# Kernel tuning notes

Measured on AMD Instinct MI355X. Metric: run time of the kernel, lower is better.

The kernel has to match this reference:

```python
import jax, jax.numpy as jnp
import numpy as np

N_NODES = 50000
N_EDGES = 800000
IN_CH = 128
HID = 32
HEADS = 4
OUT_CH = 64
NEG_SLOPE = 0.2
EPS = 1e-16


def setup_inputs() -> dict:
    key = jax.random.key(0)
    ks = jax.random.split(key, 12)
    x = jax.random.normal(ks[0], (N_NODES, IN_CH), dtype=jnp.float32)
    edge_index = jax.random.randint(ks[1], (2, N_EDGES), 0, N_NODES, dtype=jnp.int32)
    s1 = 1.0 / np.sqrt(IN_CH)
    s2 = 1.0 / np.sqrt(HEADS * HID)
    W1 = jax.random.uniform(ks[2], (IN_CH, HEADS * HID), jnp.float32, -s1, s1)
    att_src1 = jax.random.uniform(ks[3], (HEADS, HID), jnp.float32, -s2, s2)
    att_dst1 = jax.random.uniform(ks[4], (HEADS, HID), jnp.float32, -s2, s2)
    b1 = jnp.zeros((HEADS * HID,), jnp.float32)
    so = 1.0 / np.sqrt(OUT_CH)
    W2 = jax.random.uniform(ks[5], (HEADS * HID, OUT_CH), jnp.float32, -s2, s2)
    att_src2 = jax.random.uniform(ks[6], (1, OUT_CH), jnp.float32, -so, so)
    att_dst2 = jax.random.uniform(ks[7], (1, OUT_CH), jnp.float32, -so, so)
    b2 = jnp.zeros((OUT_CH,), jnp.float32)
    return {"x": x, "edge_index": edge_index, "W1": W1, "att_src1": att_src1,
            "att_dst1": att_dst1, "b1": b1, "W2": W2, "att_src2": att_src2,
            "att_dst2": att_dst2, "b2": b2}


def gat_conv(x, src, dst, W, att_src, att_dst, bias, concat):
    # x: [N, F_in], W: [F_in, H*C], att_*: [H, C], src/dst: [E'] (self loops included)
    N = x.shape[0]
    H, C = att_src.shape
    h = (x @ W).reshape(N, H, C)                       # [N, H, C]
    a_s = jnp.sum(h * att_src[None], axis=-1)          # [N, H]
    a_d = jnp.sum(h * att_dst[None], axis=-1)          # [N, H]
    alpha = jax.nn.leaky_relu(a_s[src] + a_d[dst], NEG_SLOPE)  # [E', H]
    m = jax.ops.segment_max(alpha, dst, num_segments=N)        # [N, H]
    m = jnp.where(jnp.isfinite(m), m, 0.0)
    e = jnp.exp(alpha - m[dst])                                # [E', H]
    z = jax.ops.segment_sum(e, dst, num_segments=N)            # [N, H]
    alpha = e / (z[dst] + EPS)                                 # [E', H]
    msg = h[src] * alpha[..., None]                            # [E', H, C]
    out = jax.ops.segment_sum(msg, dst, num_segments=N)        # [N, H, C]
    if concat:
        out = out.reshape(N, H * C)
    else:
        out = out.mean(axis=1)
    return out + bias


def reference(x, edge_index, W1, att_src1, att_dst1, b1, W2, att_src2, att_dst2, b2):
    N = x.shape[0]
    loops = jnp.arange(N, dtype=edge_index.dtype)
    src = jnp.concatenate([edge_index[0], loops])  # PyG add_self_loops=True
    dst = jnp.concatenate([edge_index[1], loops])
    h = gat_conv(x, src, dst, W1, att_src1, att_dst1, b1, concat=True)
    h = jax.nn.relu(h)
    h = gat_conv(h, src, dst, W2, att_src2, att_dst2, b2, concat=False)
    return jax.nn.relu(h)
```

## Files before the change

### kernel.cpp

```cpp
#include <hip/hip_runtime.h>

#define NN 50000
#define NE 800000
#define ET (NE + NN)
#define SLOPE 0.2f
#define GEPS 1e-16f
#define NBUK 196
#define BCAP 8192
#define CCHUNK 2048
#define NPB ((NE + CCHUNK - 1) / CCHUNK)
#define RBKS ((NN + 63) / 64)

typedef _Float16 f16;
typedef f16 f16x4 __attribute__((ext_vector_type(4)));
typedef f16 f16x8 __attribute__((ext_vector_type(8)));
typedef float f32x4 __attribute__((ext_vector_type(4)));

__global__ __launch_bounds__(256) void wprep_kernel(const float* __restrict__ W1,
                                                    const float* __restrict__ W2,
                                                    f16* __restrict__ wt,
                                                    int* __restrict__ bcursor) {
  int idx = blockIdx.x * 256 + threadIdx.x;
  if (idx < 16384) {
    int c = idx >> 7, k = idx & 127;
    wt[c * 128 + k] = (f16)W1[k * 128 + c];
  } else if (idx < 24576) {
    int i2 = idx - 16384;
    int c = i2 >> 7, k = i2 & 127;
    wt[16384 + c * 128 + k] = (f16)W2[k * 64 + c];
  } else if (idx - 24576 < NBUK) {
    int b = idx - 24576;
    bcursor[b] = b * BCAP;
  }
}

template <int NC, bool AF32>
__device__ __forceinline__ void gemm_body(
    f16* __restrict__ Ah, f16* __restrict__ Wh, const void* __restrict__ Av,
    const f16* __restrict__ whi, const float* __restrict__ atts,
    const float* __restrict__ attd, f16* __restrict__ Hh,
    float* __restrict__ a_s, float* __restrict__ a_d, int N, int bx, int by,
    int tid) {
  constexpr int K = 128, BM = 64, KP = K + 8;
  const int row0 = bx * BM;
  const int col0 = by * 64;
  if (AF32) {
    const float* A = (const float*)Av;
#pragma unroll
    for (int j = 0; j < 8; ++j) {
      int idx = j * 256 + tid;
      int r = idx >> 5, col = (idx & 31) << 2;
      int gr = row0 + r;
      float4 v = make_float4(0.f, 0.f, 0.f, 0.f);
      if (gr < N) v = *(const float4*)((const float*)A + (size_t)gr * K + col);
      f16x4 hv = {(f16)v.x, (f16)v.y, (f16)v.z, (f16)v.w};
      *(f16x4*)&Ah[r * KP + col] = hv;
    }
  } else {
    const f16* A = (const f16*)Av;
#pragma unroll
    for (int j = 0; j < 4; ++j) {
      int idx = j * 256 + tid;
      int r = idx >> 4, col = (idx & 15) << 3;
      int gr = row0 + r;
      f16x8 v = {};
      if (gr < N) v = *(const f16x8*)(A + (size_t)gr * K + col);
      *(f16x8*)&Ah[r * KP + col] = v;
    }
  }
#pragma unroll
  for (int j = 0; j < 4; ++j) {
    int idx = j * 256 + tid;
    int r = idx >> 4, col = (idx & 15) << 3;
    *(f16x8*)&Wh[r * KP + col] =
        *(const f16x8*)(whi + (size_t)(col0 + r) * K + col);
  }
  __syncthreads();
  const int lane = tid & 63;
  const int w = tid >> 6;
  const int lr = lane & 15;
  const int lk = (lane >> 4) << 3;
  f32x4 acc[4];
#pragma unroll
  for (int cf = 0; cf < 4; ++cf) acc[cf] = (f32x4){0.f, 0.f, 0.f, 0.f};
  const f16* arow = Ah + (w * 16 + lr) * KP + lk;
  const f16* bhrow = Wh + lr * KP + lk;
#pragma unroll
  for (int ks = 0; ks < 4; ++ks) {
    int k0 = ks * 32;
    f16x8 af = *(const f16x8*)(arow + k0);
#pragma unroll
    for (int cf = 0; cf < 4; ++cf) {
      f16x8 bh = *(const f16x8*)(bhrow + cf * 16 * KP + k0);
      acc[cf] = __builtin_amdgcn_mfma_f32_16x16x32_f16(af, bh, acc[cf], 0, 0, 0);
    }
  }
  const int rbase = row0 + w * 16 + ((lane >> 4) << 2);
#pragma unroll
  for (int cf = 0; cf < 4; ++cf) {
    int col = col0 + cf * 16 + lr;
#pragma unroll
    for (int r4 = 0; r4 < 4; ++r4) {
      int gr = rbase + r4;
      if (gr < N) Hh[(size_t)gr * NC + col] = (f16)acc[cf][r4];
    }
  }
  float asc[4], adc[4];
#pragma unroll
  for (int cf = 0; cf < 4; ++cf) {
    asc[cf] = atts[col0 + cf * 16 + lr];
    adc[cf] = attd[col0 + cf * 16 + lr];
  }
  if (NC == 128) {
#pragma unroll
    for (int m = 0; m < 2; ++m) {
#pragma unroll
      for (int r4 = 0; r4 < 4; ++r4) {
        float sp = acc[2 * m][r4] * asc[2 * m] + acc[2 * m + 1][r4] * asc[2 * m + 1];
        float dp = acc[2 * m][r4] * adc[2 * m] + acc[2 * m + 1][r4] * adc[2 * m + 1];
        sp += __shfl_xor(sp, 1); sp += __shfl_xor(sp, 2);
        sp += __shfl_xor(sp, 4); sp += __shfl_xor(sp, 8);
        dp += __shfl_xor(dp, 1); dp += __shfl_xor(dp, 2);
        dp += __shfl_xor(dp, 4); dp += __shfl_xor(dp, 8);
        int gr = rbase + r4;
        if (lr == 0 && gr < N) {
          int hd = by * 2 + m;
          a_s[gr * 4 + hd] = sp;
          a_d[gr * 4 + hd] = dp;
        }
      }
    }
  } else {
#pragma unroll
    for (int r4 = 0; r4 < 4; ++r4) {
      float sp = acc[0][r4] * asc[0] + acc[1][r4] * asc[1] +
                 acc[2][r4] * asc[2] + acc[3][r4] * asc[3];
      float dp = acc[0][r4] * adc[0] + acc[1][r4] * adc[1] +
                 acc[2][r4] * adc[2] + acc[3][r4] * adc[3];
      sp += __shfl_xor(sp, 1); sp += __shfl_xor(sp, 2);
      sp += __shfl_xor(sp, 4); sp += __shfl_xor(sp, 8);
      dp += __shfl_xor(dp, 1); dp += __shfl_xor(dp, 2);
      dp += __shfl_xor(dp, 4); dp += __shfl_xor(dp, 8);
      int gr = rbase + r4;
      if (lr == 0 && gr < N) {
        a_s[gr] = sp;
        a_d[gr] = dp;
      }
    }
  }
}

__global__ __launch_bounds__(256) void fused1_kernel(
    const int* __restrict__ src, const int* __restrict__ dst,
    int* __restrict__ bcursor, unsigned int* __restrict__ ebuf,
    const float* __restrict__ x, const f16* __restrict__ whi,
    const float* __restrict__ atts, const float* __restrict__ attd,
    f16* __restrict__ Hh, float* __restrict__ a_s, float* __restrict__ a_d,
    int N) {
  constexpr int KP = 136;
  __shared__ __align__(16) char smem[2 * 64 * KP * sizeof(f16)];
  int t = threadIdx.x;
  if (blockIdx.x < NPB) {
    int* cnt = (int*)smem;
    int* ofs = cnt + NBUK;
    int* lcur = ofs + NBUK;
    for (int i = t; i < NBUK; i += 256) {
      cnt[i] = 0;
      lcur[i] = 0;
    }
    __syncthreads();
    int base = blockIdx.x * CCHUNK;
    int nend = min(base + CCHUNK, NE);
    for (int i = base + t; i < nend; i += 256) atomicAdd(&cnt[dst[i] >> 8], 1);
    __syncthreads();
    for (int i = t; i < NBUK; i += 256)
      if (cnt[i] > 0) ofs[i] = atomicAdd(&bcursor[i], cnt[i]);
    __syncthreads();
    for (int i = base + t; i < nend; i += 256) {
      int d = dst[i];
      int s = src[i];
      int b = d >> 8;
      int p = ofs[b] + atomicAdd(&lcur[b], 1);
      ebuf[p] = ((unsigned)(d & 255) << 16) | (unsigned)s;
    }
  } else {
    int gb = blockIdx.x - NPB;
    int bx = (gb >= RBKS) ? gb - RBKS : gb;
    int by = (gb >= RBKS) ? 1 : 0;
    f16* Ah = (f16*)smem;
    f16* Wh = Ah + 64 * KP;
    gemm_body<128, true>(Ah, Wh, x, whi, atts, attd, Hh, a_s, a_d, N, bx, by, t);
  }
}

template <int NC, bool AF32>
__global__ __launch_bounds__(256) void mfma_gemm_kernel(
    const void* __restrict__ Av, const f16* __restrict__ whi,
    const float* __restrict__ atts, const float* __restrict__ attd,
    f16* __restrict__ Hh, float* __restrict__ a_s, float* __restrict__ a_d,
    int N) {
  constexpr int KP = 136;
  __shared__ f16 Ah[64 * KP];
  __shared__ f16 Wh[64 * KP];
  gemm_body<NC, AF32>(Ah, Wh, Av, whi, atts, attd, Hh, a_s, a_d, N,
                      blockIdx.x, blockIdx.y, threadIdx.x);
}

__global__ __launch_bounds__(256) void bcsr_kernel(
    const unsigned int* __restrict__ ebuf, const int* __restrict__ bcursor,
    int* __restrict__ rowptr, unsigned short* __restrict__ csr) {
  __shared__ int sc[256];
  __shared__ int deg[256];
  __shared__ int lcur[256];
  int b = blockIdx.x;
  int t = threadIdx.x;
  int nodes_t = (t < NBUK) ? min(256, NN - t * 256) : 0;
  int v = (t < NBUK) ? (bcursor[t] - t * BCAP + nodes_t) : 0;
  sc[t] = v;
  __syncthreads();
  for (int off = 1; off < 256; off <<= 1) {
    int u = (t >= off) ? sc[t - off] : 0;
    __syncthreads();
    sc[t] += u;
    __syncthreads();
  }
  int cb = (b > 0) ? sc[b - 1] : 0;
  if (b == NBUK - 1 && t == 0) rowptr[NN] = ET;
  int ebase = b * BCAP;
  int count = bcursor[b] - ebase;
  int n0 = b * 256;
  int nodes = min(256, NN - n0);
  deg[t] = 0;
  __syncthreads();
  for (int i = t; i < count; i += 256) atomicAdd(&deg[ebuf[ebase + i] >> 16], 1);
  __syncthreads();
  int myv = (t < nodes) ? (deg[t] + 1) : 0;
  __syncthreads();
  deg[t] = myv;
  __syncthreads();
  for (int off = 1; off < 256; off <<= 1) {
    int u = (t >= off) ? deg[t - off] : 0;
    __syncthreads();
    deg[t] += u;
    __syncthreads();
  }
  if (t < nodes) {
    int excl = cb + deg[t] - myv;
    rowptr[n0 + t] = excl;
    csr[excl] = (unsigned short)(n0 + t);
    lcur[t] = excl + 1;
  }
  __syncthreads();
  for (int i = t; i < count; i += 256) {
    unsigned e = ebuf[ebase + i];
    int p = atomicAdd(&lcur[e >> 16], 1);
    csr[p] = (unsigned short)(e & 0xFFFFu);
  }
}

__global__ __launch_bounds__(256) void gat1_kernel(
    const int* __restrict__ rowptr, const unsigned short* __restrict__ csr_src,
    const f16* __restrict__ h1, const float* __restrict__ as1,
    const float* __restrict__ ad1, const float* __restrict__ b1,
    f16* __restrict__ out1, int N) {
  int n = (blockIdx.x * 256 + threadIdx.x) >> 6;
  int l = threadIdx.x & 63;
  if (n >= N) return;
  int start = rowptr[n], end = rowptr[n + 1];
  int deg = end - start;
  int c = l & 15, q = l >> 4;
  int hB = c >> 2;
  float ad_b = ad1[n * 4 + hB];
  int chunk = (deg + 3) >> 2;
  int e0 = start + q * chunk;
  int ee = min(e0 + chunk, end);
  float acc[8] = {0.f, 0.f, 0.f, 0.f, 0.f, 0.f, 0.f, 0.f};
  float z = 0.f;
  {
    int sv[4];
#pragma unroll
    for (int k = 0; k < 4; ++k) {
      int ek = e0 + k;
      sv[k] = csr_src[ek < ee ? ek : start];
    }
    float av[4];
    f16x8 gv[4];
#pragma unroll
    for (int k = 0; k < 4; ++k) {
      av[k] = as1[sv[k] * 4 + hB];
      gv[k] = *(const f16x8*)(h1 + (size_t)sv[k] * 128 + 8 * c);
    }
#pragma unroll
    for (int k = 0; k < 4; ++k) {
      float a = av[k] + ad_b;
      a = (a > 0.f) ? a : SLOPE * a;
      float w = (e0 + k < ee) ? __expf(a) : 0.f;
      z += w;
#pragma unroll
      for (int j = 0; j < 8; ++j) acc[j] += w * (float)gv[k][j];
    }
  }
  if (chunk > 4) {
    int sv[4];
#pragma unroll
    for (int k = 0; k < 4; ++k) {
      int ek = e0 + 4 + k;
      sv[k] = csr_src[ek < ee ? ek : start];
    }
    float av[4];
    f16x8 gv[4];
#pragma unroll
    for (int k = 0; k < 4; ++k) {
      av[k] = as1[sv[k] * 4 + hB];
      gv[k] = *(const f16x8*)(h1 + (size_t)sv[k] * 128 + 8 * c);
    }
#pragma unroll
    for (int k = 0; k < 4; ++k) {
      float a = av[k] + ad_b;
      a = (a > 0.f) ? a : SLOPE * a;
      float w = (e0 + 4 + k < ee) ? __expf(a) : 0.f;
      z += w;
#pragma unroll
      for (int j = 0; j < 8; ++j) acc[j] += w * (float)gv[k][j];
    }
  }
  for (int e = e0 + 8; e < ee; ++e) {
    int s = csr_src[e];
    float a = as1[s * 4 + hB] + ad_b;
    a = (a > 0.f) ? a : SLOPE * a;
    float w = __expf(a);
    f16x8 g = *(const f16x8*)(h1 + (size_t)s * 128 + 8 * c);
#pragma unroll
    for (int j = 0; j < 8; ++j) acc[j] += w * (float)g[j];
    z += w;
  }
#pragma unroll
  for (int j = 0; j < 8; ++j) {
    acc[j] += __shfl_xor(acc[j], 16);
    acc[j] += __shfl_xor(acc[j], 32);
  }
  z += __shfl_xor(z, 16);
  z += __shfl_xor(z, 32);
  if (q == 0) {
    float inv = 1.f / (z + GEPS);
    float4 bb0 = *(const float4*)(b1 + 8 * c);
    float4 bb1 = *(const float4*)(b1 + 8 * c + 4);
    f16x8 o;
    o[0] = (f16)fmaxf(acc[0] * inv + bb0.x, 0.f);
    o[1] = (f16)fmaxf(acc[1] * inv + bb0.y, 0.f);
    o[2] = (f16)fmaxf(acc[2] * inv + bb0.z, 0.f);
    o[3] = (f16)fmaxf(acc[3] * inv + bb0.w, 0.f);
    o[4] = (f16)fmaxf(acc[4] * inv + bb1.x, 0.f);
    o[5] = (f16)fmaxf(acc[5] * inv + bb1.y, 0.f);
    o[6] = (f16)fmaxf(acc[6] * inv + bb1.z, 0.f);
    o[7] = (f16)fmaxf(acc[7] * inv + bb1.w, 0.f);
    *(f16x8*)(out1 + (size_t)n * 128 + 8 * c) = o;
  }
}

__global__ __launch_bounds__(256) void gat2_kernel(
    const int* __restrict__ rowptr, const unsigned short* __restrict__ csr_src,
    const f16* __restrict__ h2, const float* __restrict__ as2,
    const float* __restrict__ ad2, const float* __restrict__ b2,
    float* __restrict__ out, int N) {
  int n = (blockIdx.x * 256 + threadIdx.x) >> 6;
  int l = threadIdx.x & 63;
  if (n >= N) return;
  int start = rowptr[n], end = rowptr[n + 1];
  int deg = end - start;
  int c = l & 7, q = l >> 3;
  float ad = ad2[n];
  int chunk = (deg + 7) >> 3;
  int e0 = start + q * chunk;
  int ee = min(e0 + chunk, end);
  float acc[8] = {0.f, 0.f, 0.f, 0.f, 0.f, 0.f, 0.f, 0.f};
  float z = 0.f;
  {
    int sv[4];
#pragma unroll
    for (int k = 0; k < 4; ++k) {
      int ek = e0 + k;
      sv[k] = csr_src[ek < ee ? ek : start];
    }
    float av[4];
    f16x8 gv[4];
#pragma unroll
    for (int k = 0; k < 4; ++k) {
      av[k] = as2[sv[k]];
      gv[k] = *(const f16x8*)(h2 + (size_t)sv[k] * 64 + 8 * c);
    }
#pragma unroll
    for (int k = 0; k < 4; ++k) {
      float a = av[k] + ad;
      a = (a > 0.f) ? a : SLOPE * a;
      float w = (e0 + k < ee) ? __expf(a) : 0.f;
      z += w;
#pragma unroll
      for (int j = 0; j < 8; ++j) acc[j] += w * (float)gv[k][j];
    }
  }
  for (int e = e0 + 4; e < ee; ++e) {
    int s = csr_src[e];
    float a = as2[s] + ad;
    a = (a > 0.f) ? a : SLOPE * a;
    float w = __expf(a);
    f16x8 g = *(const f16x8*)(h2 + (size_t)s * 64 + 8 * c);
#pragma unroll
    for (int j = 0; j < 8; ++j) acc[j] += w * (float)g[j];
    z += w;
  }
#pragma unroll
  for (int j = 0; j < 8; ++j) {
    acc[j] += __shfl_xor(acc[j], 8);
    acc[j] += __shfl_xor(acc[j], 16);
    acc[j] += __shfl_xor(acc[j], 32);
  }
  z += __shfl_xor(z, 8);
  z += __shfl_xor(z, 16);
  z += __shfl_xor(z, 32);
  if (q == 0) {
    float inv = 1.f / (z + GEPS);
    float4 bb0 = *(const float4*)(b2 + 8 * c);
    float4 bb1 = *(const float4*)(b2 + 8 * c + 4);
    float4 o0, o1;
    o0.x = fmaxf(acc[0] * inv + bb0.x, 0.f);
    o0.y = fmaxf(acc[1] * inv + bb0.y, 0.f);
    o0.z = fmaxf(acc[2] * inv + bb0.z, 0.f);
    o0.w = fmaxf(acc[3] * inv + bb0.w, 0.f);
    o1.x = fmaxf(acc[4] * inv + bb1.x, 0.f);
    o1.y = fmaxf(acc[5] * inv + bb1.y, 0.f);
    o1.z = fmaxf(acc[6] * inv + bb1.z, 0.f);
    o1.w = fmaxf(acc[7] * inv + bb1.w, 0.f);
    *(float4*)(out + (size_t)n * 64 + 8 * c) = o0;
    *(float4*)(out + (size_t)n * 64 + 8 * c + 4) = o1;
  }
}

extern "C" void kernel_launch(void* const* d_in, const int* in_sizes, int n_in,
                              void* d_out, int out_size, void* d_ws, size_t ws_size,
                              hipStream_t stream) {
  const float* x = (const float*)d_in[0];
  const int* ei = (const int*)d_in[1];
  const float* W1 = (const float*)d_in[2];
  const float* att_s1 = (const float*)d_in[3];
  const float* att_d1 = (const float*)d_in[4];
  const float* b1 = (const float*)d_in[5];
  const float* W2 = (const float*)d_in[6];
  const float* att_s2 = (const float*)d_in[7];
  const float* att_d2 = (const float*)d_in[8];
  const float* b2 = (const float*)d_in[9];
  float* out = (float*)d_out;

  char* ws = (char*)d_ws;
  size_t off = 0;
  auto alloc = [&](size_t bytes) {
    off = (off + 255) & ~(size_t)255;
    void* p = ws + off;
    off += bytes;
    return p;
  };
  int* bcursor = (int*)alloc(NBUK * sizeof(int));
  unsigned int* ebuf = (unsigned int*)alloc((size_t)NBUK * BCAP * sizeof(unsigned int));
  int* rowptr = (int*)alloc((NN + 1) * sizeof(int));
  unsigned short* csr_src = (unsigned short*)alloc((size_t)ET * sizeof(unsigned short));
  f16* wt = (f16*)alloc(24576 * sizeof(f16));
  f16* h1 = (f16*)alloc((size_t)NN * 128 * sizeof(f16));
  float* as1 = (float*)alloc((size_t)NN * 4 * sizeof(float));
  float* ad1 = (float*)alloc((size_t)NN * 4 * sizeof(float));
  f16* out1h = (f16*)alloc((size_t)NN * 128 * sizeof(f16));
  f16* hh2 = h1;
  float* as2 = as1;
  float* ad2 = ad1;

  const int* src = ei;
  const int* dst = ei + NE;

  hipLaunchKernelGGL(wprep_kernel, dim3(97), dim3(256), 0, stream, W1, W2, wt,
                     bcursor);
  hipLaunchKernelGGL(fused1_kernel, dim3(NPB + 2 * RBKS), dim3(256), 0, stream, src,
                     dst, bcursor, ebuf, x, wt, att_s1, att_d1, h1, as1, ad1, NN);
  hipLaunchKernelGGL(bcsr_kernel, dim3(NBUK), dim3(256), 0, stream, ebuf, bcursor,
                     rowptr, csr_src);
  hipLaunchKernelGGL(gat1_kernel, dim3((NN + 3) / 4), dim3(256), 0, stream, rowptr,
                     csr_src, h1, as1, ad1, b1, out1h, NN);
  hipLaunchKernelGGL((mfma_gemm_kernel<64, false>), dim3(RBKS, 1), dim3(256), 0,
                     stream, out1h, wt + 16384, att_s2, att_d2, hh2, as2, ad2, NN);
  hipLaunchKernelGGL(gat2_kernel, dim3((NN + 3) / 4), dim3(256), 0, stream, rowptr,
                     csr_src, hh2, as2, ad2, b2, out, NN);
}
```

Baseline: 112.6 us.

## Drop weight-prep kernel by transposing fp32 weights inside GEMM tile loads

Removes the separate weight transpose/convert launch. Each GEMM block now reads fp32 W directly and writes it transposed as fp16 into shared memory, and the bucket cursors are zeroed with a memset, with bucket offsets added at use sites. Separately, the gat1 edge loop's second unrolled 4-edge group is split into two 2-edge groups so short rows do fewer wasted loads. The trade is one fewer kernel launch against more redundant weight conversion per block and scalar, possibly bank-conflicting shared-memory stores.

```diff
diff --git a/kernel.cpp b/kernel.cpp
--- a/kernel.cpp
+++ b/kernel.cpp
@@ -16,28 +16,10 @@
 typedef f16 f16x8 __attribute__((ext_vector_type(8)));
 typedef float f32x4 __attribute__((ext_vector_type(4)));
 
-__global__ __launch_bounds__(256) void wprep_kernel(const float* __restrict__ W1,
-                                                    const float* __restrict__ W2,
-                                                    f16* __restrict__ wt,
-                                                    int* __restrict__ bcursor) {
-  int idx = blockIdx.x * 256 + threadIdx.x;
-  if (idx < 16384) {
-    int c = idx >> 7, k = idx & 127;
-    wt[c * 128 + k] = (f16)W1[k * 128 + c];
-  } else if (idx < 24576) {
-    int i2 = idx - 16384;
-    int c = i2 >> 7, k = i2 & 127;
-    wt[16384 + c * 128 + k] = (f16)W2[k * 64 + c];
-  } else if (idx - 24576 < NBUK) {
-    int b = idx - 24576;
-    bcursor[b] = b * BCAP;
-  }
-}
-
 template <int NC, bool AF32>
 __device__ __forceinline__ void gemm_body(
     f16* __restrict__ Ah, f16* __restrict__ Wh, const void* __restrict__ Av,
-    const f16* __restrict__ whi, const float* __restrict__ atts,
+    const float* __restrict__ W, const float* __restrict__ atts,
     const float* __restrict__ attd, f16* __restrict__ Hh,
     float* __restrict__ a_s, float* __restrict__ a_d, int N, int bx, int by,
     int tid) {
@@ -69,11 +51,14 @@
     }
   }
 #pragma unroll
-  for (int j = 0; j < 4; ++j) {
+  for (int j = 0; j < 8; ++j) {
     int idx = j * 256 + tid;
-    int r = idx >> 4, col = (idx & 15) << 3;
-    *(f16x8*)&Wh[r * KP + col] =
-        *(const f16x8*)(whi + (size_t)(col0 + r) * K + col);
+    int k = idx >> 4, c4 = (idx & 15) << 2;
+    float4 v = *(const float4*)(W + (size_t)k * NC + col0 + c4);
+    Wh[(c4 + 0) * KP + k] = (f16)v.x;
+    Wh[(c4 + 1) * KP + k] = (f16)v.y;
+    Wh[(c4 + 2) * KP + k] = (f16)v.z;
+    Wh[(c4 + 3) * KP + k] = (f16)v.w;
   }
   __syncthreads();
   const int lane = tid & 63;
@@ -153,7 +138,7 @@
 __global__ __launch_bounds__(256) void fused1_kernel(
     const int* __restrict__ src, const int* __restrict__ dst,
     int* __restrict__ bcursor, unsigned int* __restrict__ ebuf,
-    const float* __restrict__ x, const f16* __restrict__ whi,
+    const float* __restrict__ x, const float* __restrict__ W1,
     const float* __restrict__ atts, const float* __restrict__ attd,
     f16* __restrict__ Hh, float* __restrict__ a_s, float* __restrict__ a_d,
     int N) {
@@ -180,7 +165,7 @@
       int d = dst[i];
       int s = src[i];
       int b = d >> 8;
-      int p = ofs[b] + atomicAdd(&lcur[b], 1);
+      int p = b * BCAP + ofs[b] + atomicAdd(&lcur[b], 1);
       ebuf[p] = ((unsigned)(d & 255) << 16) | (unsigned)s;
     }
   } else {
@@ -189,20 +174,20 @@
     int by = (gb >= RBKS) ? 1 : 0;
     f16* Ah = (f16*)smem;
     f16* Wh = Ah + 64 * KP;
-    gemm_body<128, true>(Ah, Wh, x, whi, atts, attd, Hh, a_s, a_d, N, bx, by, t);
+    gemm_body<128, true>(Ah, Wh, x, W1, atts, attd, Hh, a_s, a_d, N, bx, by, t);
   }
 }
 
 template <int NC, bool AF32>
 __global__ __launch_bounds__(256) void mfma_gemm_kernel(
-    const void* __restrict__ Av, const f16* __restrict__ whi,
+    const void* __restrict__ Av, const float* __restrict__ W,
     const float* __restrict__ atts, const float* __restrict__ attd,
     f16* __restrict__ Hh, float* __restrict__ a_s, float* __restrict__ a_d,
     int N) {
   constexpr int KP = 136;
   __shared__ f16 Ah[64 * KP];
   __shared__ f16 Wh[64 * KP];
-  gemm_body<NC, AF32>(Ah, Wh, Av, whi, atts, attd, Hh, a_s, a_d, N,
+  gemm_body<NC, AF32>(Ah, Wh, Av, W, atts, attd, Hh, a_s, a_d, N,
                       blockIdx.x, blockIdx.y, threadIdx.x);
 }
 
@@ -215,7 +200,7 @@
   int b = blockIdx.x;
   int t = threadIdx.x;
   int nodes_t = (t < NBUK) ? min(256, NN - t * 256) : 0;
-  int v = (t < NBUK) ? (bcursor[t] - t * BCAP + nodes_t) : 0;
+  int v = (t < NBUK) ? (bcursor[t] + nodes_t) : 0;
   sc[t] = v;
   __syncthreads();
   for (int off = 1; off < 256; off <<= 1) {
@@ -227,7 +212,7 @@
   int cb = (b > 0) ? sc[b - 1] : 0;
   if (b == NBUK - 1 && t == 0) rowptr[NN] = ET;
   int ebase = b * BCAP;
-  int count = bcursor[b] - ebase;
+  int count = bcursor[b];
   int n0 = b * 256;
   int nodes = min(256, NN - n0);
   deg[t] = 0;
@@ -301,24 +286,48 @@
     }
   }
   if (chunk > 4) {
-    int sv[4];
-#pragma unroll
-    for (int k = 0; k < 4; ++k) {
+    int sv[2];
+#pragma unroll
+    for (int k = 0; k < 2; ++k) {
       int ek = e0 + 4 + k;
       sv[k] = csr_src[ek < ee ? ek : start];
     }
-    float av[4];
-    f16x8 gv[4];
-#pragma unroll
-    for (int k = 0; k < 4; ++k) {
+    float av[2];
+    f16x8 gv[2];
+#pragma unroll
+    for (int k = 0; k < 2; ++k) {
       av[k] = as1[sv[k] * 4 + hB];
       gv[k] = *(const f16x8*)(h1 + (size_t)sv[k] * 128 + 8 * c);
     }
 #pragma unroll
-    for (int k = 0; k < 4; ++k) {
+    for (int k = 0; k < 2; ++k) {
       float a = av[k] + ad_b;
       a = (a > 0.f) ? a : SLOPE * a;
       float w = (e0 + 4 + k < ee) ? __expf(a) : 0.f;
+      z += w;
+#pragma unroll
+      for (int j = 0; j < 8; ++j) acc[j] += w * (float)gv[k][j];
+    }
+  }
+  if (chunk > 6) {
+    int sv[2];
+#pragma unroll
+    for (int k = 0; k < 2; ++k) {
+      int ek = e0 + 6 + k;
+      sv[k] = csr_src[ek < ee ? ek : start];
+    }
+    float av[2];
+    f16x8 gv[2];
+#pragma unroll
+    for (int k = 0; k < 2; ++k) {
+      av[k] = as1[sv[k] * 4 + hB];
+      gv[k] = *(const f16x8*)(h1 + (size_t)sv[k] * 128 + 8 * c);
+    }
+#pragma unroll
+    for (int k = 0; k < 2; ++k) {
+      float a = av[k] + ad_b;
+      a = (a > 0.f) ? a : SLOPE * a;
+      float w = (e0 + 6 + k < ee) ? __expf(a) : 0.f;
       z += w;
 #pragma unroll
       for (int j = 0; j < 8; ++j) acc[j] += w * (float)gv[k][j];
@@ -463,7 +472,6 @@
   unsigned int* ebuf = (unsigned int*)alloc((size_t)NBUK * BCAP * sizeof(unsigned int));
   int* rowptr = (int*)alloc((NN + 1) * sizeof(int));
   unsigned short* csr_src = (unsigned short*)alloc((size_t)ET * sizeof(unsigned short));
-  f16* wt = (f16*)alloc(24576 * sizeof(f16));
   f16* h1 = (f16*)alloc((size_t)NN * 128 * sizeof(f16));
   float* as1 = (float*)alloc((size_t)NN * 4 * sizeof(float));
   float* ad1 = (float*)alloc((size_t)NN * 4 * sizeof(float));
@@ -475,16 +483,15 @@
   const int* src = ei;
   const int* dst = ei + NE;
 
-  hipLaunchKernelGGL(wprep_kernel, dim3(97), dim3(256), 0, stream, W1, W2, wt,
-                     bcursor);
+  hipMemsetAsync(bcursor, 0, NBUK * sizeof(int), stream);
   hipLaunchKernelGGL(fused1_kernel, dim3(NPB + 2 * RBKS), dim3(256), 0, stream, src,
-                     dst, bcursor, ebuf, x, wt, att_s1, att_d1, h1, as1, ad1, NN);
+                     dst, bcursor, ebuf, x, W1, att_s1, att_d1, h1, as1, ad1, NN);
   hipLaunchKernelGGL(bcsr_kernel, dim3(NBUK), dim3(256), 0, stream, ebuf, bcursor,
                      rowptr, csr_src);
   hipLaunchKernelGGL(gat1_kernel, dim3((NN + 3) / 4), dim3(256), 0, stream, rowptr,
                      csr_src, h1, as1, ad1, b1, out1h, NN);
   hipLaunchKernelGGL((mfma_gemm_kernel<64, false>), dim3(RBKS, 1), dim3(256), 0,
-                     stream, out1h, wt + 16384, att_s2, att_d2, hh2, as2, ad2, NN);
+                     stream, out1h, W2, att_s2, att_d2, hh2, as2, ad2, NN);
   hipLaunchKernelGGL(gat2_kernel, dim3((NN + 3) / 4), dim3(256), 0, stream, rowptr,
                      csr_src, hh2, as2, ad2, b2, out, NN);
 }
```

After: 119.0 us. 5.6% more time.
